# Kernel optimization log

Hardware: AMD Instinct MI355X
Metric: run time of the kernel (lower is better)

## Reference

```python
import jax, jax.numpy as jnp
import numpy as np

EMBED = 768
HEADS = 12
HEAD_DIM = EMBED // HEADS
HIDDEN = 4 * EMBED
B, N = 8, 1024
EPS = 1e-5


def layernorm(x, g, b):
    mu = jnp.mean(x, axis=-1, keepdims=True)
    var = jnp.var(x, axis=-1, keepdims=True)
    return (x - mu) * jax.lax.rsqrt(var + EPS) * g + b


def setup_inputs() -> dict:
    key = jax.random.key(0)
    ks = jax.random.split(key, 8)
    s_qkv = 1.0 / np.sqrt(EMBED)
    s_fc1 = 1.0 / np.sqrt(EMBED)
    s_fc2 = 1.0 / np.sqrt(HIDDEN)
    return {
        "x": jax.random.normal(ks[0], (B, N, EMBED), dtype=jnp.float32),
        "ln1_g": jnp.ones((EMBED,), jnp.float32),
        "ln1_b": jnp.zeros((EMBED,), jnp.float32),
        "qkv_w": jax.random.uniform(ks[1], (3 * EMBED, EMBED), jnp.float32, -s_qkv, s_qkv),
        "qkv_b": jnp.zeros((3 * EMBED,), jnp.float32),
        "proj_w": jax.random.uniform(ks[2], (EMBED, EMBED), jnp.float32, -s_qkv, s_qkv),
        "proj_b": jnp.zeros((EMBED,), jnp.float32),
        "ln2_g": jnp.ones((EMBED,), jnp.float32),
        "ln2_b": jnp.zeros((EMBED,), jnp.float32),
        "fc1_w": jax.random.uniform(ks[3], (HIDDEN, EMBED), jnp.float32, -s_fc1, s_fc1),
        "fc1_b": jnp.zeros((HIDDEN,), jnp.float32),
        "fc2_w": jax.random.uniform(ks[4], (EMBED, HIDDEN), jnp.float32, -s_fc2, s_fc2),
        "fc2_b": jnp.zeros((EMBED,), jnp.float32),
    }


def reference(x, ln1_g, ln1_b, qkv_w, qkv_b, proj_w, proj_b,
              ln2_g, ln2_b, fc1_w, fc1_b, fc2_w, fc2_b):
    b, n, d = x.shape
    # --- attention sublayer ---
    h = layernorm(x, ln1_g, ln1_b)
    qkv = h @ qkv_w.T + qkv_b                      # [b,n,3d]
    qkv = qkv.reshape(b, n, 3, HEADS, HEAD_DIM).transpose(2, 0, 3, 1, 4)
    q, k, v = qkv[0], qkv[1], qkv[2]               # [b,h,n,hd]
    scores = jnp.einsum('bhqd,bhkd->bhqk', q, k) * (HEAD_DIM ** -0.5)
    attn = jax.nn.softmax(scores, axis=-1)
    ctx = jnp.einsum('bhqk,bhkd->bhqd', attn, v)   # [b,h,n,hd]
    ctx = ctx.transpose(0, 2, 1, 3).reshape(b, n, d)
    x = x + (ctx @ proj_w.T + proj_b)
    # --- MLP sublayer ---
    h = layernorm(x, ln2_g, ln2_b)
    h = jax.nn.gelu(h @ fc1_w.T + fc1_b, approximate=False)
    x = x + (h @ fc2_w.T + fc2_b)
    return x
```

## Files before the change

### kernel.cpp

```cpp
#include <hip/hip_runtime.h>
#include <cstdint>

typedef __bf16 bf16_t;
typedef __attribute__((ext_vector_type(8))) __bf16 bf16x8;
typedef __attribute__((ext_vector_type(4))) __bf16 bf16x4;
typedef __attribute__((ext_vector_type(4))) float f32x4;

#define MFMA16(a, b, c) __builtin_amdgcn_mfma_f32_16x16x32_bf16((a), (b), (c), 0, 0, 0)

__device__ inline void gll16(const bf16_t* g, bf16_t* lds) {
    __builtin_amdgcn_global_load_lds(
        (const __attribute__((address_space(1))) uint32_t*)g,
        (__attribute__((address_space(3))) uint32_t*)lds, 16, 0, 0);
}

__global__ __launch_bounds__(256) void cvt4_kernel(const float* __restrict__ s0, bf16_t* __restrict__ d0,
                                                   const float* __restrict__ s1, bf16_t* __restrict__ d1,
                                                   const float* __restrict__ s2, bf16_t* __restrict__ d2,
                                                   const float* __restrict__ s3, bf16_t* __restrict__ d3) {
    const int blk = blockIdx.x;
    const float* s; bf16_t* d; int base;
    if (blk < 864)       { s = s0; d = d0; base = blk; }
    else if (blk < 1152) { s = s1; d = d1; base = blk - 864; }
    else if (blk < 2304) { s = s2; d = d2; base = blk - 1152; }
    else                 { s = s3; d = d3; base = blk - 2304; }
    const int i = (base * 256 + threadIdx.x) * 8;
    const float4* sp = (const float4*)(s + i);
    float4 a = sp[0], b = sp[1];
    bf16x8 o;
    o[0] = (bf16_t)a.x; o[1] = (bf16_t)a.y; o[2] = (bf16_t)a.z; o[3] = (bf16_t)a.w;
    o[4] = (bf16_t)b.x; o[5] = (bf16_t)b.y; o[6] = (bf16_t)b.z; o[7] = (bf16_t)b.w;
    *(bf16x8*)(d + i) = o;
}

__global__ __launch_bounds__(256) void ln_kernel(const float* __restrict__ x,
                                                 const float* __restrict__ gw,
                                                 const float* __restrict__ bw,
                                                 bf16_t* __restrict__ out) {
    const int row  = blockIdx.x * 4 + (threadIdx.x >> 6);
    const int lane = threadIdx.x & 63;
    const float4* xr = (const float4*)(x + (long)row * 768);
    float4 v[3];
    float s = 0.f, q = 0.f;
#pragma unroll
    for (int j = 0; j < 3; ++j) {
        v[j] = xr[j * 64 + lane];
        s += v[j].x + v[j].y + v[j].z + v[j].w;
        q += v[j].x * v[j].x + v[j].y * v[j].y + v[j].z * v[j].z + v[j].w * v[j].w;
    }
#pragma unroll
    for (int off = 32; off > 0; off >>= 1) {
        s += __shfl_xor(s, off);
        q += __shfl_xor(q, off);
    }
    const float mu = s * (1.0f / 768.0f);
    const float rs = rsqrtf(q * (1.0f / 768.0f) - mu * mu + 1e-5f);
#pragma unroll
    for (int j = 0; j < 3; ++j) {
        float4 g4 = ((const float4*)gw)[j * 64 + lane];
        float4 b4 = ((const float4*)bw)[j * 64 + lane];
        bf16x4 o;
        o[0] = (bf16_t)((v[j].x - mu) * rs * g4.x + b4.x);
        o[1] = (bf16_t)((v[j].y - mu) * rs * g4.y + b4.y);
        o[2] = (bf16_t)((v[j].z - mu) * rs * g4.z + b4.z);
        o[3] = (bf16_t)((v[j].w - mu) * rs * g4.w + b4.w);
        *(bf16x4*)(out + (long)row * 768 + (j * 64 + lane) * 4) = o;
    }
}

template <int MODE, int NC, int RPX>
__global__ __launch_bounds__(256) void gemm_bt(const bf16_t* __restrict__ A,
                                               const bf16_t* __restrict__ Bw,
                                               const float* __restrict__ bias,
                                               bf16_t* __restrict__ outb,
                                               bf16_t* __restrict__ o1,
                                               bf16_t* __restrict__ o2,
                                               int Nn, int K) {
    __shared__ __align__(16) bf16_t As[128 * 32];
    __shared__ __align__(16) bf16_t Bs[128 * 32];
    const int id = blockIdx.x;
    const int xcd = id & 7, sblk = id >> 3;
    const int tn = (sblk % NC) * 128;
    const int tm = (xcd * RPX + sblk / NC) * 128;
    const int w = threadIdx.x >> 6, l = threadIdx.x & 63;
    const int quad = l >> 4, r16 = l & 15;
    const int wm = (w >> 1) * 64, wn = (w & 1) * 64;
    f32x4 acc[4][4] = {};
    const bf16_t* ga = A  + (long)(tm + w * 32 + (l >> 2)) * K + (l & 3) * 8;
    const bf16_t* gb = Bw + (long)(tn + w * 32 + (l >> 2)) * K + (l & 3) * 8;
    bf16_t* la = As + w * 1024;
    bf16_t* lb = Bs + w * 1024;

    for (int k0 = 0; k0 < K; k0 += 32) {
        gll16(ga + k0,            la);
        gll16(ga + 16 * K + k0,   la + 512);
        gll16(gb + k0,            lb);
        gll16(gb + 16 * K + k0,   lb + 512);
        __syncthreads();
        bf16x8 af[4], bfr[4];
#pragma unroll
        for (int i = 0; i < 4; ++i) {
            af[i]  = *(const bf16x8*)&As[(wm + i * 16 + r16) * 32 + quad * 8];
            bfr[i] = *(const bf16x8*)&Bs[(wn + i * 16 + r16) * 32 + quad * 8];
        }
#pragma unroll
        for (int i = 0; i < 4; ++i)
#pragma unroll
            for (int j = 0; j < 4; ++j)
                acc[i][j] = MFMA16(af[i], bfr[j], acc[i][j]);
        __syncthreads();
    }
#pragma unroll
    for (int i = 0; i < 4; ++i) {
        const int r0 = tm + wm + i * 16 + quad * 4;
#pragma unroll
        for (int j = 0; j < 4; ++j) {
            const int c = tn + wn + j * 16 + r16;
            const float bv = bias[c];
            if (MODE == 0) {
                const int b = r0 >> 10, n0 = r0 & 1023;
                const int sect = c / 768;
                const int cw = c - sect * 768;
                const int h = cw >> 6, d = cw & 63;
                const long hb = (long)(b * 12 + h);
                if (sect == 2) {
                    bf16x4 o;
#pragma unroll
                    for (int rr = 0; rr < 4; ++rr) o[rr] = (bf16_t)(acc[i][j][rr] + bv);
                    *(bf16x4*)(o2 + (hb * 64 + d) * 1024 + n0) = o;
                } else {
                    bf16_t* dst = (sect == 0 ? outb : o1) + hb * 65536 + (long)n0 * 64 + d;
#pragma unroll
                    for (int rr = 0; rr < 4; ++rr) dst[rr * 64] = (bf16_t)(acc[i][j][rr] + bv);
                }
            } else {
#pragma unroll
                for (int rr = 0; rr < 4; ++rr) {
                    const long idx = (long)(r0 + rr) * Nn + c;
                    const float v = acc[i][j][rr] + bv;
                    outb[idx] = (bf16_t)(0.5f * v * (1.0f + erff(v * 0.70710678118654752f)));
                }
            }
        }
    }
}

__global__ __launch_bounds__(256) void gemm_res64(const bf16_t* __restrict__ A,
                                                  const bf16_t* __restrict__ Bw,
                                                  const float* __restrict__ bias,
                                                  const float* __restrict__ res,
                                                  float* __restrict__ outf,
                                                  int Nn, int K) {
    __shared__ __align__(16) bf16_t As[64 * 32];
    __shared__ __align__(16) bf16_t Bs[128 * 32];
    const int id = blockIdx.x;
    const int xcd = id & 7, sblk = id >> 3;
    const int tn = (sblk % 6) * 128;
    const int tm = (xcd * 16 + sblk / 6) * 64;
    const int w = threadIdx.x >> 6, l = threadIdx.x & 63;
    const int quad = l >> 4, r16 = l & 15;
    const int wm = (w >> 1) * 32, wn = (w & 1) * 64;
    f32x4 acc[2][4] = {};
    const bf16_t* ga = A  + (long)(tm + w * 16 + (l >> 2)) * K + (l & 3) * 8;
    const bf16_t* gb = Bw + (long)(tn + w * 32 + (l >> 2)) * K + (l & 3) * 8;
    bf16_t* la = As + w * 512;
    bf16_t* lb = Bs + w * 1024;

    for (int k0 = 0; k0 < K; k0 += 32) {
        gll16(ga + k0,            la);
        gll16(gb + k0,            lb);
        gll16(gb + 16 * K + k0,   lb + 512);
        __syncthreads();
        bf16x8 af[2], bfr[4];
#pragma unroll
        for (int i = 0; i < 2; ++i)
            af[i]  = *(const bf16x8*)&As[(wm + i * 16 + r16) * 32 + quad * 8];
#pragma unroll
        for (int j = 0; j < 4; ++j)
            bfr[j] = *(const bf16x8*)&Bs[(wn + j * 16 + r16) * 32 + quad * 8];
#pragma unroll
        for (int i = 0; i < 2; ++i)
#pragma unroll
            for (int j = 0; j < 4; ++j)
                acc[i][j] = MFMA16(af[i], bfr[j], acc[i][j]);
        __syncthreads();
    }
#pragma unroll
    for (int i = 0; i < 2; ++i) {
        const int r0 = tm + wm + i * 16 + quad * 4;
#pragma unroll
        for (int j = 0; j < 4; ++j) {
            const int c = tn + wn + j * 16 + r16;
            const float bv = bias[c];
#pragma unroll
            for (int rr = 0; rr < 4; ++rr) {
                const long idx = (long)(r0 + rr) * Nn + c;
                outf[idx] = res[idx] + acc[i][j][rr] + bv;
            }
        }
    }
}

__global__ __launch_bounds__(256, 3) void attn_kernel(const bf16_t* __restrict__ qh,
                                                      const bf16_t* __restrict__ kh,
                                                      const bf16_t* __restrict__ vt,
                                                      bf16_t* __restrict__ ctx) {
    __shared__ __align__(16) bf16_t Ks[128 * 72];
    __shared__ __align__(16) bf16_t Vt[64 * 136];
    __shared__ __align__(16) bf16_t Ps[4 * 16 * 136];
    const int w = threadIdx.x >> 6, l = threadIdx.x & 63;
    const int quad = l >> 4, r16 = l & 15;
    const int bh = blockIdx.x, qt = blockIdx.y;
    const bf16_t* qp = qh + (long)bh * 65536;
    const bf16_t* kp = kh + (long)bh * 65536;
    const bf16_t* vp = vt + (long)bh * 65536;
    const int q0 = qt * 128 + w * 32;
    const float SC = 0.18033688011f;

    bf16x8 qf[2][2];
#pragma unroll
    for (int mt = 0; mt < 2; ++mt)
#pragma unroll
        for (int kq = 0; kq < 2; ++kq)
            qf[mt][kq] = *(const bf16x8*)(qp + (long)(q0 + mt * 16 + r16) * 64 + kq * 32 + quad * 8);

    float lsum[2][4] = {};
    f32x4 oacc[2][4] = {};

    for (int kt = 0; kt < 8; ++kt) {
        const int kb = kt * 128;
#pragma unroll
        for (int c = 0; c < 4; ++c) {
            const int cc = threadIdx.x + c * 256;
            const int row = cc >> 3, cg = cc & 7;
            *(bf16x8*)&Ks[row * 72 + cg * 8] =
                *(const bf16x8*)(kp + (long)(kb + row) * 64 + cg * 8);
        }
#pragma unroll
        for (int c = 0; c < 4; ++c) {
            const int cc = threadIdx.x + c * 256;
            const int d = cc >> 4, ck = cc & 15;
            *(bf16x8*)&Vt[d * 136 + ck * 8] =
                *(const bf16x8*)(vp + (long)d * 1024 + kb + ck * 8);
        }
        __syncthreads();

        bf16x8 kf[8][2];
#pragma unroll
        for (int nt = 0; nt < 8; ++nt) {
            kf[nt][0] = *(const bf16x8*)&Ks[(nt * 16 + r16) * 72 + quad * 8];
            kf[nt][1] = *(const bf16x8*)&Ks[(nt * 16 + r16) * 72 + 32 + quad * 8];
        }

        bf16_t* pw = Ps + w * 16 * 136;
#pragma unroll
        for (int mt = 0; mt < 2; ++mt) {
            f32x4 s[8] = {};
#pragma unroll
            for (int nt = 0; nt < 8; ++nt) {
                s[nt] = MFMA16(qf[mt][0], kf[nt][0], s[nt]);
                s[nt] = MFMA16(qf[mt][1], kf[nt][1], s[nt]);
            }
#pragma unroll
            for (int nt = 0; nt < 8; ++nt)
#pragma unroll
                for (int rr = 0; rr < 4; ++rr) {
                    const float p = exp2f(s[nt][rr] * SC);
                    lsum[mt][rr] += p;
                    pw[(quad * 4 + rr) * 136 + nt * 16 + r16] = (bf16_t)p;
                }
#pragma unroll
            for (int kc = 0; kc < 4; ++kc) {
                bf16x8 pf = *(const bf16x8*)&pw[r16 * 136 + kc * 32 + quad * 8];
#pragma unroll
                for (int dt = 0; dt < 4; ++dt) {
                    bf16x8 vf = *(const bf16x8*)&Vt[(dt * 16 + r16) * 136 + kc * 32 + quad * 8];
                    oacc[mt][dt] = MFMA16(pf, vf, oacc[mt][dt]);
                }
            }
        }
        __syncthreads();
    }
#pragma unroll
    for (int mt = 0; mt < 2; ++mt)
#pragma unroll
        for (int rr = 0; rr < 4; ++rr) {
#pragma unroll
            for (int off = 1; off < 16; off <<= 1)
                lsum[mt][rr] += __shfl_xor(lsum[mt][rr], off);
        }
    const int b = bh / 12, h = bh % 12;
    const long tb = (long)b * 1024;
#pragma unroll
    for (int mt = 0; mt < 2; ++mt)
#pragma unroll
        for (int dt = 0; dt < 4; ++dt)
#pragma unroll
            for (int rr = 0; rr < 4; ++rr) {
                const int qrow = q0 + mt * 16 + quad * 4 + rr;
                const int d = dt * 16 + r16;
                const float v = oacc[mt][dt][rr] / lsum[mt][rr];
                ctx[(tb + qrow) * 768 + h * 64 + d] = (bf16_t)v;
            }
}

extern "C" void kernel_launch(void* const* d_in, const int* in_sizes, int n_in,
                              void* d_out, int out_size, void* d_ws, size_t ws_size,
                              hipStream_t stream) {
    const float* x      = (const float*)d_in[0];
    const float* ln1_g  = (const float*)d_in[1];
    const float* ln1_b  = (const float*)d_in[2];
    const float* qkv_w  = (const float*)d_in[3];
    const float* qkv_b  = (const float*)d_in[4];
    const float* proj_w = (const float*)d_in[5];
    const float* proj_b = (const float*)d_in[6];
    const float* ln2_g  = (const float*)d_in[7];
    const float* ln2_b  = (const float*)d_in[8];
    const float* fc1_w  = (const float*)d_in[9];
    const float* fc1_b  = (const float*)d_in[10];
    const float* fc2_w  = (const float*)d_in[11];
    const float* fc2_b  = (const float*)d_in[12];

    char* p = (char*)d_ws;
    bf16_t* wqkv  = (bf16_t*)p; p += (size_t)2304 * 768 * 2;
    bf16_t* wproj = (bf16_t*)p; p += (size_t)768 * 768 * 2;
    bf16_t* wfc1  = (bf16_t*)p; p += (size_t)3072 * 768 * 2;
    bf16_t* wfc2  = (bf16_t*)p; p += (size_t)768 * 3072 * 2;
    bf16_t* h1    = (bf16_t*)p; p += (size_t)8192 * 768 * 2;
    bf16_t* qhb   = (bf16_t*)p; p += (size_t)96 * 1024 * 64 * 2;
    bf16_t* khb   = (bf16_t*)p; p += (size_t)96 * 1024 * 64 * 2;
    bf16_t* vtb   = (bf16_t*)p; p += (size_t)96 * 64 * 1024 * 2;
    bf16_t* ctx   = (bf16_t*)p; p += (size_t)8192 * 768 * 2;
    float*  x2    = (float*)p;  p += (size_t)8192 * 768 * 4;
    bf16_t* h2    = (bf16_t*)p; p += (size_t)8192 * 768 * 2;
    bf16_t* a1    = (bf16_t*)p; p += (size_t)8192 * 3072 * 2;

    cvt4_kernel<<<3456, 256, 0, stream>>>(qkv_w, wqkv, proj_w, wproj, fc1_w, wfc1, fc2_w, wfc2);

    ln_kernel<<<2048, 256, 0, stream>>>(x, ln1_g, ln1_b, h1);
    gemm_bt<0, 18, 8><<<1152, 256, 0, stream>>>(h1, wqkv, qkv_b, qhb, khb, vtb, 2304, 768);
    attn_kernel<<<dim3(96, 8), 256, 0, stream>>>(qhb, khb, vtb, ctx);
    gemm_res64<<<768, 256, 0, stream>>>(ctx, wproj, proj_b, x, x2, 768, 768);
    ln_kernel<<<2048, 256, 0, stream>>>(x2, ln2_g, ln2_b, h2);
    gemm_bt<2, 24, 8><<<1536, 256, 0, stream>>>(h2, wfc1, fc1_b, a1, nullptr, nullptr, 3072, 768);
    gemm_res64<<<768, 256, 0, stream>>>(a1, wfc2, fc2_b, x2, (float*)d_out, 768, 3072);
}
```

Measured before the change: 403.9 us.

## Stage GEMM epilogues through LDS, tanh GELU, and load attention K/V directly

The GEMM epilogues now write accumulator tiles into a small per-wave LDS buffer and then emit 16-byte coalesced global stores, replacing the scattered scalar stores. The residual GEMM also reads the residual with float4 loads. GELU switches from erf to a tanh/sigmoid approximation built on exp2f, which cuts math cost but changes numerics slightly. The attention kernel drops the shared K/V staging and its block barriers, loading K and V fragments straight from global memory into registers, which trades LDS reuse across waves for redundant global traffic and higher register pressure.

```diff
diff --git a/kernel.cpp b/kernel.cpp
--- a/kernel.cpp
+++ b/kernel.cpp
@@ -12,6 +12,11 @@
     __builtin_amdgcn_global_load_lds(
         (const __attribute__((address_space(1))) uint32_t*)g,
         (__attribute__((address_space(3))) uint32_t*)lds, 16, 0, 0);
+}
+
+__device__ inline float gelu_f(float v) {
+    const float u = v + 0.044715f * v * v * v;
+    return v / (1.0f + exp2f(-2.3022038f * u));
 }
 
 __global__ __launch_bounds__(256) void cvt4_kernel(const float* __restrict__ s0, bf16_t* __restrict__ d0,
@@ -78,6 +83,7 @@
                                                int Nn, int K) {
     __shared__ __align__(16) bf16_t As[128 * 32];
     __shared__ __align__(16) bf16_t Bs[128 * 32];
+    __shared__ __align__(16) bf16_t Ts[4 * 16 * 72];
     const int id = blockIdx.x;
     const int xcd = id & 7, sblk = id >> 3;
     const int tn = (sblk % NC) * 128;
@@ -110,36 +116,63 @@
                 acc[i][j] = MFMA16(af[i], bfr[j], acc[i][j]);
         __syncthreads();
     }
-#pragma unroll
-    for (int i = 0; i < 4; ++i) {
-        const int r0 = tm + wm + i * 16 + quad * 4;
-#pragma unroll
-        for (int j = 0; j < 4; ++j) {
-            const int c = tn + wn + j * 16 + r16;
-            const float bv = bias[c];
-            if (MODE == 0) {
+
+    bf16_t* tw = Ts + w * 16 * 72;
+    if (MODE == 0) {
+        const int sect = (tn + wn) / 768;
+        const int cwb  = tn + wn - sect * 768;
+        const int h    = cwb >> 6;
+        if (sect == 2) {
+#pragma unroll
+            for (int i = 0; i < 4; ++i) {
+                const int r0 = tm + wm + i * 16 + quad * 4;
                 const int b = r0 >> 10, n0 = r0 & 1023;
-                const int sect = c / 768;
-                const int cw = c - sect * 768;
-                const int h = cw >> 6, d = cw & 63;
-                const long hb = (long)(b * 12 + h);
-                if (sect == 2) {
+#pragma unroll
+                for (int j = 0; j < 4; ++j) {
+                    const int d = j * 16 + r16;
+                    const float bv = bias[tn + wn + j * 16 + r16];
                     bf16x4 o;
 #pragma unroll
                     for (int rr = 0; rr < 4; ++rr) o[rr] = (bf16_t)(acc[i][j][rr] + bv);
-                    *(bf16x4*)(o2 + (hb * 64 + d) * 1024 + n0) = o;
-                } else {
-                    bf16_t* dst = (sect == 0 ? outb : o1) + hb * 65536 + (long)n0 * 64 + d;
-#pragma unroll
-                    for (int rr = 0; rr < 4; ++rr) dst[rr * 64] = (bf16_t)(acc[i][j][rr] + bv);
+                    *(bf16x4*)(o2 + ((long)(b * 12 + h) * 64 + d) * 1024 + n0) = o;
                 }
-            } else {
-#pragma unroll
-                for (int rr = 0; rr < 4; ++rr) {
-                    const long idx = (long)(r0 + rr) * Nn + c;
-                    const float v = acc[i][j][rr] + bv;
-                    outb[idx] = (bf16_t)(0.5f * v * (1.0f + erff(v * 0.70710678118654752f)));
+            }
+        } else {
+            bf16_t* dstbuf = (sect == 0 ? outb : o1);
+#pragma unroll
+            for (int i = 0; i < 4; ++i) {
+#pragma unroll
+                for (int j = 0; j < 4; ++j) {
+                    const float bv = bias[tn + wn + j * 16 + r16];
+#pragma unroll
+                    for (int rr = 0; rr < 4; ++rr)
+                        tw[(quad * 4 + rr) * 72 + j * 16 + r16] = (bf16_t)(acc[i][j][rr] + bv);
                 }
+                const int tok = tm + wm + i * 16 + (l >> 2);
+                const int b = tok >> 10, n0 = tok & 1023;
+                const long base = (long)(b * 12 + h) * 65536 + (long)n0 * 64;
+#pragma unroll
+                for (int it = 0; it < 2; ++it) {
+                    bf16x8 vv = *(const bf16x8*)&tw[(l >> 2) * 72 + (l & 3) * 8 + it * 32];
+                    *(bf16x8*)(dstbuf + base + (l & 3) * 8 + it * 32) = vv;
+                }
+            }
+        }
+    } else {
+#pragma unroll
+        for (int i = 0; i < 4; ++i) {
+#pragma unroll
+            for (int j = 0; j < 4; ++j) {
+                const float bv = bias[tn + wn + j * 16 + r16];
+#pragma unroll
+                for (int rr = 0; rr < 4; ++rr)
+                    tw[(quad * 4 + rr) * 72 + j * 16 + r16] = (bf16_t)gelu_f(acc[i][j][rr] + bv);
+            }
+            const int grow = tm + wm + i * 16 + (l >> 2);
+#pragma unroll
+            for (int it = 0; it < 2; ++it) {
+                bf16x8 vv = *(const bf16x8*)&tw[(l >> 2) * 72 + (l & 3) * 8 + it * 32];
+                *(bf16x8*)(outb + (long)grow * Nn + tn + wn + (l & 3) * 8 + it * 32) = vv;
             }
         }
     }
@@ -153,6 +186,7 @@
                                                   int Nn, int K) {
     __shared__ __align__(16) bf16_t As[64 * 32];
     __shared__ __align__(16) bf16_t Bs[128 * 32];
+    __shared__ __align__(16) float  Tf[4 * 16 * 68];
     const int id = blockIdx.x;
     const int xcd = id & 7, sblk = id >> 3;
     const int tn = (sblk % 6) * 128;
@@ -185,18 +219,26 @@
                 acc[i][j] = MFMA16(af[i], bfr[j], acc[i][j]);
         __syncthreads();
     }
+    float* tf = Tf + w * 16 * 68;
 #pragma unroll
     for (int i = 0; i < 2; ++i) {
-        const int r0 = tm + wm + i * 16 + quad * 4;
 #pragma unroll
         for (int j = 0; j < 4; ++j) {
-            const int c = tn + wn + j * 16 + r16;
-            const float bv = bias[c];
-#pragma unroll
-            for (int rr = 0; rr < 4; ++rr) {
-                const long idx = (long)(r0 + rr) * Nn + c;
-                outf[idx] = res[idx] + acc[i][j][rr] + bv;
-            }
+            const float bv = bias[tn + wn + j * 16 + r16];
+#pragma unroll
+            for (int rr = 0; rr < 4; ++rr)
+                tf[(quad * 4 + rr) * 68 + j * 16 + r16] = acc[i][j][rr] + bv;
+        }
+        const int grow = tm + wm + i * 16 + (l >> 2);
+#pragma unroll
+        for (int it = 0; it < 4; ++it) {
+            const int gcol = tn + wn + (l & 3) * 4 + it * 16;
+            f32x4 vv = *(const f32x4*)&tf[(l >> 2) * 68 + (l & 3) * 4 + it * 16];
+            const float4 rv = *(const float4*)(res + (long)grow * Nn + gcol);
+            float4 ov;
+            ov.x = rv.x + vv[0]; ov.y = rv.y + vv[1];
+            ov.z = rv.z + vv[2]; ov.w = rv.w + vv[3];
+            *(float4*)(outf + (long)grow * Nn + gcol) = ov;
         }
     }
 }
@@ -205,8 +247,6 @@
                                                       const bf16_t* __restrict__ kh,
                                                       const bf16_t* __restrict__ vt,
                                                       bf16_t* __restrict__ ctx) {
-    __shared__ __align__(16) bf16_t Ks[128 * 72];
-    __shared__ __align__(16) bf16_t Vt[64 * 136];
     __shared__ __align__(16) bf16_t Ps[4 * 16 * 136];
     const int w = threadIdx.x >> 6, l = threadIdx.x & 63;
     const int quad = l >> 4, r16 = l & 15;
@@ -226,33 +266,25 @@
 
     float lsum[2][4] = {};
     f32x4 oacc[2][4] = {};
+    bf16_t* pw = Ps + w * 16 * 136;
 
     for (int kt = 0; kt < 8; ++kt) {
         const int kb = kt * 128;
-#pragma unroll
-        for (int c = 0; c < 4; ++c) {
-            const int cc = threadIdx.x + c * 256;
-            const int row = cc >> 3, cg = cc & 7;
-            *(bf16x8*)&Ks[row * 72 + cg * 8] =
-                *(const bf16x8*)(kp + (long)(kb + row) * 64 + cg * 8);
-        }
-#pragma unroll
-        for (int c = 0; c < 4; ++c) {
-            const int cc = threadIdx.x + c * 256;
-            const int d = cc >> 4, ck = cc & 15;
-            *(bf16x8*)&Vt[d * 136 + ck * 8] =
-                *(const bf16x8*)(vp + (long)d * 1024 + kb + ck * 8);
-        }
-        __syncthreads();
-
         bf16x8 kf[8][2];
 #pragma unroll
         for (int nt = 0; nt < 8; ++nt) {
-            kf[nt][0] = *(const bf16x8*)&Ks[(nt * 16 + r16) * 72 + quad * 8];
-            kf[nt][1] = *(const bf16x8*)&Ks[(nt * 16 + r16) * 72 + 32 + quad * 8];
-        }
-
-        bf16_t* pw = Ps + w * 16 * 136;
+            const bf16_t* kr = kp + (long)(kb + nt * 16 + r16) * 64 + quad * 8;
+            kf[nt][0] = *(const bf16x8*)kr;
+            kf[nt][1] = *(const bf16x8*)(kr + 32);
+        }
+        bf16x8 vf[4][4];
+#pragma unroll
+        for (int dt = 0; dt < 4; ++dt) {
+            const bf16_t* vr = vp + (long)(dt * 16 + r16) * 1024 + kb + quad * 8;
+#pragma unroll
+            for (int kc = 0; kc < 4; ++kc)
+                vf[kc][dt] = *(const bf16x8*)(vr + kc * 32);
+        }
 #pragma unroll
         for (int mt = 0; mt < 2; ++mt) {
             f32x4 s[8] = {};
@@ -273,13 +305,10 @@
             for (int kc = 0; kc < 4; ++kc) {
                 bf16x8 pf = *(const bf16x8*)&pw[r16 * 136 + kc * 32 + quad * 8];
 #pragma unroll
-                for (int dt = 0; dt < 4; ++dt) {
-                    bf16x8 vf = *(const bf16x8*)&Vt[(dt * 16 + r16) * 136 + kc * 32 + quad * 8];
-                    oacc[mt][dt] = MFMA16(pf, vf, oacc[mt][dt]);
-                }
-            }
-        }
-        __syncthreads();
+                for (int dt = 0; dt < 4; ++dt)
+                    oacc[mt][dt] = MFMA16(pf, vf[kc][dt], oacc[mt][dt]);
+            }
+        }
     }
 #pragma unroll
     for (int mt = 0; mt < 2; ++mt)
```

Result: slower. 435.9 us (+7.9%).
